# Kernel tuning notes

Hardware: AMD Instinct MI355X
Metric: run time of the kernel (lower is better)

Reference implementation:

```python
import jax, jax.numpy as jnp
import numpy as np

TOPK = 32
NUM_PT = 8192
NUM_KP = 8
HW = 19200


def _conv3(x, w, b):
    # x: [1, C, N], w: [O, C, 3] -> [1, O, N] (padding=1)
    y = jax.lax.conv_general_dilated(x, w, (1,), [(1, 1)],
                                     dimension_numbers=('NCH', 'OIH', 'NCH'))
    return y + b[None, :, None]


def setup_inputs() -> dict:
    key = jax.random.key(0)
    ks = jax.random.split(key, 64)

    def p(i, *shape):
        return (jax.random.normal(ks[i], shape, dtype=jnp.float32) * 0.05)

    inp = {
        'seg': jax.random.uniform(ks[0], (1, NUM_PT), dtype=jnp.float32),
        'img': jax.random.normal(ks[1], (1, 32, HW), dtype=jnp.float32),
        'cloud': jax.random.normal(ks[2], (1, NUM_PT, 3), dtype=jnp.float32),
        't': jax.random.normal(ks[3], (1, 3), dtype=jnp.float32),
        'choose': jax.random.randint(ks[4], (1, 1, NUM_PT), 0, HW),
        # Pseudo3DConv params (all 1x1 conv1d == channel matmul)
        'pconv1_w': p(5, 64, 3),    'pconv1_b': p(6, 64),
        'pconv2_w': p(7, 128, 64),  'pconv2_b': p(8, 128),
        'conv1_w': p(9, 64, 32),    'conv1_b': p(10, 64),
        'conv2_w': p(11, 128, 64),  'conv2_b': p(12, 128),
        'psconv1_w': p(13, 256, 128), 'psconv1_b': p(14, 256),
        'psconv2_w': p(15, 128, 256), 'psconv2_b': p(16, 128),
        'final_w': p(17, 128, 416), 'final_b': p(18, 128),
        # heads
        'seg1_w': p(19, 64, 128, 3), 'seg1_b': p(20, 64),
        'seg2_w': p(21, 32, 64),     'seg2_b': p(22, 32),
        'seg3_w': p(23, 1, 32),      'seg3_b': p(24, 1),
        'dis1_w': p(25, 64, 128, 3), 'dis1_b': p(26, 64),
        'dis2_w': p(27, 32, 64),     'dis2_b': p(28, 32),
        'dis3_w': p(29, 1, 32),      'dis3_b': p(30, 1),
        'lin1_w': p(31, 90, 128),    'lin1_b': p(32, 90),
        'lin2_w': p(33, 64, 90),     'lin2_b': p(34, 64),
        'lin3_w': p(35, 3 * NUM_KP, 64), 'lin3_b': p(36, 3 * NUM_KP),
    }
    return inp


def reference(seg, img, cloud, t, choose,
              pconv1_w, pconv1_b, pconv2_w, pconv2_b,
              conv1_w, conv1_b, conv2_w, conv2_b,
              psconv1_w, psconv1_b, psconv2_w, psconv2_b,
              final_w, final_b,
              seg1_w, seg1_b, seg2_w, seg2_b, seg3_w, seg3_b,
              dis1_w, dis1_b, dis2_w, dis2_b, dis3_w, dis3_b,
              lin1_w, lin1_b, lin2_w, lin2_b, lin3_w, lin3_b):
    lrelu = jax.nn.leaky_relu  # slope 0.01, same as torch default
    N = NUM_PT

    # gather per-point image features at chosen pixels: [N, 32]
    feat = jnp.take(img[0], choose[0, 0], axis=1).T
    c = cloud[0]  # [N, 3]

    # ---- KNN (self included, as in knn_cuda) ----
    d2 = jnp.sum((c[:, None, :] - c[None, :, :]) ** 2, axis=-1)  # [N, N]
    _, idx = jax.lax.top_k(-d2, TOPK)  # [N, K] nearest neighbors

    # ---- point-feature MLP (pconv1 -> lrelu -> pconv2) ----
    pf = lrelu(c @ pconv1_w.T + pconv1_b) @ pconv2_w.T + pconv2_b  # [N, 128]

    # ---- vectorized per-point neighbor gather + MLP + weighted maxpool ----
    nf = feat[idx]    # [N, K, 32]
    npf = pf[idx]     # [N, K, 128]
    npos = c[idx]     # [N, K, 3]
    w = jax.nn.softmax(-jnp.linalg.norm(c[:, None, :] - npos, axis=-1), axis=1)  # [N, K]

    f = lrelu(nf @ conv1_w.T + conv1_b) @ conv2_w.T + conv2_b          # [N, K, 128]
    fp = lrelu(npf @ psconv1_w.T + psconv1_b) @ psconv2_w.T + psconv2_b  # [N, K, 128]
    f = jnp.max(f * w[..., None], axis=1)    # [N, 128]
    fp = jnp.max(fp * w[..., None], axis=1)  # [N, 128]

    # final2 = [fp | img_feat], final1 = [f | cloud_feat] -> cat -> [N, 416]
    final = jnp.concatenate([fp, feat, f, pf], axis=1)
    fused = lrelu(final) @ final_w.T + final_b  # [N, 128]
    fused = fused.T[None]  # [1, 128, N]

    def pw(x, w_, b_):  # 1x1 conv1d on [1, C, N]
        return jnp.einsum('oc,bcn->bon', w_, x) + b_[None, :, None]

    # segmentation head
    h = lrelu(_conv3(fused, seg1_w, seg1_b))
    seg_pre = pw(lrelu(pw(h, seg2_w, seg2_b)), seg3_w, seg3_b).reshape(1, N)

    # distance-to-center weighting (norm along coord dim, softmax over points)
    dis_center = jax.nn.softmax(
        jnp.linalg.norm(cloud - (-t)[:, None, :], axis=2), axis=1)  # [1, N]

    # distance head (on unweighted fused features, matching torch op order)
    h = lrelu(_conv3(fused, dis1_w, dis1_b))
    dis_pre = pw(lrelu(pw(h, dis2_w, dis2_b)), dis3_w, dis3_b).reshape(1, N)

    # weight fused features by center distance and segmentation, sum-pool
    fused = fused * dis_center[:, None, :] * seg[:, None, :]
    g = jnp.sum(fused, axis=2)  # [1, 128]

    kp = lrelu(g @ lin1_w.T + lin1_b)
    kp = lrelu(kp @ lin2_w.T + lin2_b)
    keypoints = (kp @ lin3_w.T + lin3_b).reshape(1, NUM_KP, 3)
    return keypoints, dis_pre, dis_center, seg_pre
```

## Files before the change

### kernel.cpp

```cpp
#include <hip/hip_runtime.h>
#include <math.h>

#define NPT 8192
#define HWIMG 19200
#define KCAP 128

using short8 = __attribute__((ext_vector_type(8))) short;
using short4v = __attribute__((ext_vector_type(4))) short;
using f32x4  = __attribute__((ext_vector_type(4))) float;

__device__ __forceinline__ float lrelu(float x) { return x > 0.f ? x : 0.01f * x; }
__device__ __forceinline__ unsigned short f2bf(float v) {
  unsigned u = __float_as_uint(v);
  return (unsigned short)((u + 0x7fffu + ((u >> 16) & 1u)) >> 16);
}
__device__ __forceinline__ float bf2f(unsigned short h) {
  return __uint_as_float(((unsigned)h) << 16);
}
__device__ __forceinline__ void split2(float v, unsigned short& h, unsigned short& l) {
  h = f2bf(v);
  l = f2bf(v - bf2f(h));
}
__device__ __forceinline__ void mfma3(f32x4& acc, short8 ah, short8 al, short8 wh, short8 wl) {
  acc = __builtin_amdgcn_mfma_f32_16x16x32_bf16(ah, wh, acc, 0, 0, 0);
  acc = __builtin_amdgcn_mfma_f32_16x16x32_bf16(al, wh, acc, 0, 0, 0);
  acc = __builtin_amdgcn_mfma_f32_16x16x32_bf16(ah, wl, acc, 0, 0, 0);
}

__device__ __forceinline__ int swz(int o, int k, int Kc) {
  return ((((o >> 4) * Kc + (k >> 5)) << 6) + (((k >> 3) & 3) << 4) + (o & 15)) * 8 + (k & 7);
}

#define OFF_PCONV2  0
#define OFF_CONV1   8192
#define OFF_CONV2   10240
#define OFF_PSCONV1 18432
#define OFF_PSCONV2 51200
#define OFF_FINAL   83968
#define OFF_W3      137216
#define OFF_W2P     186368

#define S_C4    NPT
#define S_G     129
#define S_BIASC 128
#define S_B2C   64
#define S_FEAT  (NPT*32)
#define S_W3    49152
#define S_W2P   8192
#define S_WSPL  OFF_W3
#define PREP_TOTAL (S_C4 + S_G + S_BIASC + S_B2C + S_FEAT + S_W3 + S_W2P + S_WSPL)
__global__ void k_prep(const float* __restrict__ cloud, const int* __restrict__ choose,
                       const float* __restrict__ img,
                       const float* __restrict__ seg1_w, const float* __restrict__ dis1_w,
                       const float* __restrict__ seg1_b, const float* __restrict__ dis1_b,
                       const float* __restrict__ seg2_w, const float* __restrict__ dis2_w,
                       const float* __restrict__ seg2_b, const float* __restrict__ dis2_b,
                       const float* __restrict__ pconv2_w, const float* __restrict__ conv1_w,
                       const float* __restrict__ conv2_w, const float* __restrict__ psconv1_w,
                       const float* __restrict__ psconv2_w, const float* __restrict__ final_w,
                       float* __restrict__ c4, float* __restrict__ g,
                       float* __restrict__ biasc, float* __restrict__ bias2c,
                       float* __restrict__ feat,
                       unsigned short* __restrict__ feat_h, unsigned short* __restrict__ feat_l,
                       unsigned short* __restrict__ Wh, unsigned short* __restrict__ Wl) {
  int j = blockIdx.x * blockDim.x + threadIdx.x;
  if (j < S_C4) {
    float x = cloud[j*3+0], y = cloud[j*3+1], z = cloud[j*3+2];
    float4 v; v.x = x; v.y = y; v.z = z; v.w = x*x + y*y + z*z;
    ((float4*)c4)[j] = v;
    return;
  }
  j -= S_C4;
  if (j < S_G) { g[j] = 0.f; return; }
  j -= S_G;
  if (j < S_BIASC) { biasc[j] = (j < 64) ? seg1_b[j] : dis1_b[j-64]; return; }
  j -= S_BIASC;
  if (j < S_B2C) { bias2c[j] = (j < 32) ? seg2_b[j] : dis2_b[j-32]; return; }
  j -= S_B2C;
  if (j < S_FEAT) {
    int n = j >> 5, ch = j & 31;
    float v = img[ch*HWIMG + choose[n]];
    feat[j] = v;
    unsigned short hh, ll; split2(v, hh, ll);
    int d = swz(n, ch, 1);
    feat_h[d] = hh; feat_l[d] = ll;
    return;
  }
  j -= S_FEAT;
  if (j < S_W3) {
    int h = j / 24576, r = j - h*24576, o = r / 384, k = r - o*384;
    int t = k >> 7, c = k & 127;
    float v = (h ? dis1_w : seg1_w)[o*384 + c*3 + t];
    unsigned short hh, ll; split2(v, hh, ll);
    int d = OFF_W3 + swz(h*64 + o, k, 12);
    Wh[d] = hh; Wl[d] = ll;
    return;
  }
  j -= S_W3;
  if (j < S_W2P) {
    int o = j >> 7, c = j & 127;
    float v = 0.f;
    if (o < 32) { if (c < 64) v = seg2_w[o*64 + c]; }
    else        { if (c >= 64) v = dis2_w[(o-32)*64 + (c-64)]; }
    unsigned short hh, ll; split2(v, hh, ll);
    int d = OFF_W2P + swz(o, c, 4);
    Wh[d] = hh; Wl[d] = ll;
    return;
  }
  j -= S_W2P;
  if (j < S_WSPL) {
    float v; int d;
    if (j < OFF_CONV1) {
      int o = j >> 6, k = j & 63;
      v = pconv2_w[j]; d = OFF_PCONV2 + swz(o, k, 2);
    } else if (j < OFF_CONV2) {
      int jj = j - OFF_CONV1, o = jj >> 5, k = jj & 31;
      v = conv1_w[jj]; d = OFF_CONV1 + swz(o, k, 1);
    } else if (j < OFF_PSCONV1) {
      int jj = j - OFF_CONV2, o = jj >> 6, k = jj & 63;
      v = conv2_w[jj]; d = OFF_CONV2 + swz(o, k, 2);
    } else if (j < OFF_PSCONV2) {
      int jj = j - OFF_PSCONV1, o = jj >> 7, k = jj & 127;
      v = psconv1_w[jj]; d = OFF_PSCONV1 + swz(o, k, 4);
    } else if (j < OFF_FINAL) {
      int jj = j - OFF_PSCONV2, o = jj >> 8, k = jj & 255;
      v = psconv2_w[jj]; d = OFF_PSCONV2 + swz(o, k, 8);
    } else {
      int jj = j - OFF_FINAL, o = jj / 416, k = jj - o*416;
      v = final_w[jj]; d = OFF_FINAL + swz(o, k, 13);
    }
    unsigned short hh, ll; split2(v, hh, ll);
    Wh[d] = hh; Wl[d] = ll;
  }
}

__device__ __forceinline__ unsigned bsort32u(unsigned key, int lane) {
#pragma unroll
  for (int k = 2; k <= 64; k <<= 1) {
#pragma unroll
    for (int j = k >> 1; j > 0; j >>= 1) {
      unsigned o = __shfl_xor(key, j, 64);
      bool keepmin = (((lane & j) == 0) == ((lane & k) == 0));
      key = ((o < key) == keepmin) ? o : key;
    }
  }
  return key;
}
__device__ __forceinline__ unsigned long long bsort64(unsigned long long key, int lane) {
#pragma unroll
  for (int k = 2; k <= 64; k <<= 1) {
#pragma unroll
    for (int j = k >> 1; j > 0; j >>= 1) {
      unsigned long long o = __shfl_xor(key, j, 64);
      bool keepmin = (((lane & j) == 0) == ((lane & k) == 0));
      bool omin = o < key;
      key = (omin == keepmin) ? o : key;
    }
  }
  return key;
}
__device__ __forceinline__ unsigned long long bmerge64(unsigned long long key, int lane) {
#pragma unroll
  for (int j = 32; j > 0; j >>= 1) {
    unsigned long long o = __shfl_xor(key, j, 64);
    bool keepmin = ((lane & j) == 0);
    bool omin = o < key;
    key = (omin == keepmin) ? o : key;
  }
  return key;
}

#define MEGA_GRID 3073
__global__ __launch_bounds__(256) void k_mega(const float4* __restrict__ c4,
                                              int* __restrict__ idxo, float* __restrict__ wo,
                                              const float* __restrict__ cloud,
                                              const float* __restrict__ tvec,
                                              float* __restrict__ dc,
                                              const float* __restrict__ pconv1_w, const float* __restrict__ pconv1_b,
                                              const float* __restrict__ pconv2_b, const float* __restrict__ psconv1_b,
                                              const float* __restrict__ psconv2_b,
                                              const unsigned short* __restrict__ feat_h,
                                              const unsigned short* __restrict__ feat_l,
                                              const float* __restrict__ conv1_b, const float* __restrict__ conv2_b,
                                              const unsigned short* __restrict__ Wh,
                                              const unsigned short* __restrict__ Wl,
                                              float* __restrict__ pf, float* __restrict__ Yfp,
                                              float* __restrict__ Yf) {
  __shared__ __align__(16) char smem[16384];
  int tid = threadIdx.x, lane = tid & 63, w = tid >> 6;
  int mr = lane & 15, q = lane >> 4;
  if (blockIdx.x > 2048) {
    unsigned short* sh_h = (unsigned short*)smem;
    unsigned short* sh_l = (unsigned short*)(smem + 8192);
    int cb = blockIdx.x - 2049;
    if (cb < 512) {
      int m0 = cb * 16;
      float4 cp = c4[m0 + mr];
      short8 ah0, al0, ah1, al1;
#pragma unroll
      for (int j = 0; j < 8; ++j) {
        int c0 = q*8 + j, c1 = 32 + q*8 + j;
        float v0 = lrelu(fmaf(cp.x, pconv1_w[c0*3+0], fmaf(cp.y, pconv1_w[c0*3+1],
                          fmaf(cp.z, pconv1_w[c0*3+2], pconv1_b[c0]))));
        float v1 = lrelu(fmaf(cp.x, pconv1_w[c1*3+0], fmaf(cp.y, pconv1_w[c1*3+1],
                          fmaf(cp.z, pconv1_w[c1*3+2], pconv1_b[c1]))));
        unsigned short hh, ll;
        split2(v0, hh, ll); ah0[j] = (short)hh; al0[j] = (short)ll;
        split2(v1, hh, ll); ah1[j] = (short)hh; al1[j] = (short)ll;
      }
      f32x4 acc[2];
#pragma unroll
      for (int t = 0; t < 2; ++t) { f32x4 z = {0.f,0.f,0.f,0.f}; acc[t] = z; }
      const unsigned short* W2h = Wh + OFF_PCONV2;
      const unsigned short* W2l = Wl + OFF_PCONV2;
#pragma unroll
      for (int tt = 0; tt < 2; ++tt) {
        int t1 = 2*w + tt;
        int w0 = ((t1*2 + 0)*64 + lane)*8, w1 = ((t1*2 + 1)*64 + lane)*8;
        mfma3(acc[tt], ah0, al0, *(const short8*)(W2h + w0), *(const short8*)(W2l + w0));
        mfma3(acc[tt], ah1, al1, *(const short8*)(W2h + w1), *(const short8*)(W2l + w1));
      }
#pragma unroll
      for (int tt = 0; tt < 2; ++tt) {
        int t1 = 2*w + tt, n = t1*16 + mr;
        float b = pconv2_b[n];
        int ks2 = t1 >> 1, q2 = (t1 & 1)*2 + (mr >> 3), jd = mr & 7;
#pragma unroll
        for (int r = 0; r < 4; ++r) {
          int row = q*4 + r;
          float v = acc[tt][r] + b;
          pf[(size_t)(m0+row)*128 + n] = v;
          unsigned short hh, ll; split2(v, hh, ll);
          int p = ((ks2*16 + row)*4 + q2)*8 + jd;
          sh_h[p] = hh; sh_l[p] = ll;
        }
      }
      __syncthreads();
      f32x4 acc3[2];
#pragma unroll
      for (int t = 0; t < 2; ++t) { f32x4 z = {0.f,0.f,0.f,0.f}; acc3[t] = z; }
      const unsigned short* W3h = Wh + OFF_PSCONV1;
      const unsigned short* W3l = Wl + OFF_PSCONV1;
      const unsigned short* W4h = Wh + OFF_PSCONV2;
      const unsigned short* W4l = Wl + OFF_PSCONV2;
#pragma unroll
      for (int h = 0; h < 2; ++h) {
        f32x4 acc2[2];
#pragma unroll
        for (int t = 0; t < 2; ++t) { f32x4 z = {0.f,0.f,0.f,0.f}; acc2[t] = z; }
#pragma unroll
        for (int ks = 0; ks < 4; ++ks) {
          int ap = ((ks*16 + mr)*4 + q)*8;
          short8 ah = *(const short8*)&sh_h[ap];
          short8 al = *(const short8*)&sh_l[ap];
#pragma unroll
          for (int tt = 0; tt < 2; ++tt) {
            int ts = h*8 + 2*w + tt;
            int wb = ((ts*4 + ks)*64 + lane)*8;
            mfma3(acc2[tt], ah, al, *(const short8*)(W3h + wb), *(const short8*)(W3l + wb));
          }
        }
#pragma unroll
        for (int tt = 0; tt < 2; ++tt) {
          int tl = 2*w + tt;
          int n = h*128 + tl*16 + mr;
          float b = psconv1_b[n];
          int ks3 = tl >> 1, q3 = (tl & 1)*2 + (mr >> 3), jd = mr & 7;
#pragma unroll
          for (int r = 0; r < 4; ++r) {
            int row = q*4 + r;
            float v = lrelu(acc2[tt][r] + b);
            unsigned short hh, ll; split2(v, hh, ll);
            int p = 2048 + ((ks3*16 + row)*4 + q3)*8 + jd;
            sh_h[p] = hh; sh_l[p] = ll;
          }
        }
        __syncthreads();
#pragma unroll
        for (int ks = 0; ks < 4; ++ks) {
          int ap = 2048 + ((ks*16 + mr)*4 + q)*8;
          short8 ah = *(const short8*)&sh_h[ap];
          short8 al = *(const short8*)&sh_l[ap];
#pragma unroll
          for (int tt = 0; tt < 2; ++tt) {
            int wb = (((2*w+tt)*8 + h*4 + ks)*64 + lane)*8;
            mfma3(acc3[tt], ah, al, *(const short8*)(W4h + wb), *(const short8*)(W4l + wb));
          }
        }
        __syncthreads();
      }
#pragma unroll
      for (int tt = 0; tt < 2; ++tt) {
        int n = (2*w+tt)*16 + mr;
        float b = psconv2_b[n];
#pragma unroll
        for (int r = 0; r < 4; ++r)
          Yfp[(size_t)(m0 + q*4 + r)*128 + n] = acc3[tt][r] + b;
      }
    } else {
      int m0 = (cb - 512) * 16;
      int ab = ((m0 >> 4)*64 + lane)*8;
      short8 ah = *(const short8*)(feat_h + ab);
      short8 al = *(const short8*)(feat_l + ab);
      f32x4 acc = {0.f,0.f,0.f,0.f};
      const unsigned short* W1h = Wh + OFF_CONV1;
      const unsigned short* W1l = Wl + OFF_CONV1;
      {
        int wb = (w*64 + lane)*8;
        mfma3(acc, ah, al, *(const short8*)(W1h + wb), *(const short8*)(W1l + wb));
      }
      {
        int n = w*16 + mr;
        float b = conv1_b[n];
        int ks2 = n >> 5, q2 = (n >> 3) & 3, jd = mr & 7;
#pragma unroll
        for (int r = 0; r < 4; ++r) {
          int row = q*4 + r;
          float v = lrelu(acc[r] + b);
          unsigned short hh, ll; split2(v, hh, ll);
          int p = ((ks2*16 + row)*4 + q2)*8 + jd;
          sh_h[p] = hh; sh_l[p] = ll;
        }
      }
      __syncthreads();
      f32x4 acc2[2];
#pragma unroll
      for (int t = 0; t < 2; ++t) { f32x4 z = {0.f,0.f,0.f,0.f}; acc2[t] = z; }
      const unsigned short* W2h = Wh + OFF_CONV2;
      const unsigned short* W2l = Wl + OFF_CONV2;
#pragma unroll
      for (int ks = 0; ks < 2; ++ks) {
        int ap = ((ks*16 + mr)*4 + q)*8;
        short8 a2 = *(const short8*)&sh_h[ap];
        short8 a2l = *(const short8*)&sh_l[ap];
#pragma unroll
        for (int tt = 0; tt < 2; ++tt) {
          int wb = (((2*w+tt)*2 + ks)*64 + lane)*8;
          mfma3(acc2[tt], a2, a2l, *(const short8*)(W2h + wb), *(const short8*)(W2l + wb));
        }
      }
#pragma unroll
      for (int tt = 0; tt < 2; ++tt) {
        int n = (2*w+tt)*16 + mr;
        float b = conv2_b[n];
#pragma unroll
        for (int r = 0; r < 4; ++r)
          Yf[(size_t)(m0 + q*4 + r)*128 + n] = acc2[tt][r] + b;
      }
    }
    return;
  }
  if (blockIdx.x == 2048) {
    float* sred = (float*)smem;
    float tx = tvec[0], ty = tvec[1], tz = tvec[2];
    float v[32];
    float m = -INFINITY;
#pragma unroll
    for (int i2 = 0; i2 < 32; ++i2) {
      int n = i2*256 + tid;
      float ax = cloud[n*3+0] + tx, ay = cloud[n*3+1] + ty, az = cloud[n*3+2] + tz;
      v[i2] = sqrtf(ax*ax + ay*ay + az*az);
      m = fmaxf(m, v[i2]);
    }
#pragma unroll
    for (int o = 1; o < 64; o <<= 1) m = fmaxf(m, __shfl_xor(m, o, 64));
    if (lane == 0) sred[w] = m;
    __syncthreads();
    m = fmaxf(fmaxf(sred[0], sred[1]), fmaxf(sred[2], sred[3]));
    __syncthreads();
    float s = 0.f;
#pragma unroll
    for (int i2 = 0; i2 < 32; ++i2) { v[i2] = expf(v[i2] - m); s += v[i2]; }
#pragma unroll
    for (int o = 1; o < 64; o <<= 1) s += __shfl_xor(s, o, 64);
    if (lane == 0) sred[w] = s;
    __syncthreads();
    s = sred[0] + sred[1] + sred[2] + sred[3];
#pragma unroll
    for (int i2 = 0; i2 < 32; ++i2) dc[i2*256 + tid] = v[i2] / s;
    return;
  }
  float (*smin)[256] = (float(*)[256])smem;
  float* sTv = (float*)(smem + 4096);
  int*   scnt = (int*)(smem + 4112);
  float (*sd)[KCAP] = (float(*)[KCAP])(smem + 4128);
  int   (*sj)[KCAP] = (int(*)[KCAP])(smem + 6176);
  int q0 = blockIdx.x * 4;
  float4 p0 = c4[q0], p1 = c4[q0+1], p2 = c4[q0+2], p3 = c4[q0+3];
  float p0x = -2.f*p0.x, p0y = -2.f*p0.y, p0z = -2.f*p0.z;
  float p1x = -2.f*p1.x, p1y = -2.f*p1.y, p1z = -2.f*p1.z;
  float p2x = -2.f*p2.x, p2y = -2.f*p2.y, p2z = -2.f*p2.z;
  float p3x = -2.f*p3.x, p3y = -2.f*p3.y, p3z = -2.f*p3.z;
#define DDOT(PX,PY,PZ,PW,CJ) fmaf(PX,(CJ).x, fmaf(PY,(CJ).y, fmaf(PZ,(CJ).z, PW + (CJ).w)))
  float m0 = INFINITY, m1 = INFINITY, m2 = INFINITY, m3 = INFINITY;
  for (int t = 0; t < 32; t += 2) {
    float4 ca = c4[t*256 + tid];
    float4 cb = c4[t*256 + 256 + tid];
    float a0 = DDOT(p0x,p0y,p0z,p0.w,ca), b0 = DDOT(p0x,p0y,p0z,p0.w,cb);
    float a1 = DDOT(p1x,p1y,p1z,p1.w,ca), b1 = DDOT(p1x,p1y,p1z,p1.w,cb);
    float a2 = DDOT(p2x,p2y,p2z,p2.w,ca), b2 = DDOT(p2x,p2y,p2z,p2.w,cb);
    float a3 = DDOT(p3x,p3y,p3z,p3.w,ca), b3 = DDOT(p3x,p3y,p3z,p3.w,cb);
    m0 = fminf(m0, fminf(a0, b0));
    m1 = fminf(m1, fminf(a1, b1));
    m2 = fminf(m2, fminf(a2, b2));
    m3 = fminf(m3, fminf(a3, b3));
  }
  smin[0][tid] = m0; smin[1][tid] = m1; smin[2][tid] = m2; smin[3][tid] = m3;
  if (tid < 4) scnt[tid] = 0;
  __syncthreads();
  {
    float4 vv = *(const float4*)&smin[w][lane*4];
    float m4 = fmaxf(fminf(fminf(vv.x, vv.y), fminf(vv.z, vv.w)), 0.f);
    unsigned key = bsort32u(__float_as_uint(m4), lane);
    float T = __uint_as_float(__shfl(key, 31, 64));
    if (lane == 0) sTv[w] = T * (1.f + 2e-5f) + 4e-5f;
  }
  __syncthreads();
  float T0 = sTv[0], T1 = sTv[1], T2 = sTv[2], T3 = sTv[3];
  for (int t = 0; t < 32; ++t) {
    int j = t*256 + tid;
    float4 cj = c4[j];
    float d;
#define APPEND(Q, P) { \
    float dx_ = (P).x-cj.x, dy_ = (P).y-cj.y, dz_ = (P).z-cj.z; \
    float de_ = dx_*dx_ + dy_*dy_ + dz_*dz_; \
    int p_ = atomicAdd(&scnt[Q],1); if (p_ < KCAP) { sd[Q][p_] = de_; sj[Q][p_] = j; } }
    d = DDOT(p0x,p0y,p0z,p0.w,cj); if (d <= T0) APPEND(0, p0);
    d = DDOT(p1x,p1y,p1z,p1.w,cj); if (d <= T1) APPEND(1, p1);
    d = DDOT(p2x,p2y,p2z,p2.w,cj); if (d <= T2) APPEND(2, p2);
    d = DDOT(p3x,p3y,p3z,p3.w,cj); if (d <= T3) APPEND(3, p3);
  }
  __syncthreads();
  int M = scnt[w]; if (M > KCAP) M = KCAP;
  unsigned long long key = (lane < M)
      ? (((unsigned long long)__float_as_uint(sd[w][lane]) << 32) | (unsigned)sj[w][lane])
      : ~0ull;
  key = bsort64(key, lane);
  for (int base = 64; base < M; base += 64) {
    unsigned long long nk = (base + lane < M)
        ? (((unsigned long long)__float_as_uint(sd[w][base+lane]) << 32) | (unsigned)sj[w][base+lane])
        : ~0ull;
    nk = bsort64(nk, lane);
    nk = __shfl_xor(nk, 63, 64);
    key = key < nk ? key : nk;
    key = bmerge64(key, lane);
  }
  float dsel = __uint_as_float((unsigned)(key >> 32));
  int   jsel = (int)(unsigned)(key & 0xffffffffu);
  float v = -sqrtf(dsel);
  float mx = v;
#pragma unroll
  for (int o = 1; o < 32; o <<= 1) mx = fmaxf(mx, __shfl_xor(mx, o, 64));
  float e = expf(v - mx);
  float s = e;
#pragma unroll
  for (int o = 1; o < 32; o <<= 1) s += __shfl_xor(s, o, 64);
  if (lane < 32) {
    int qd = q0 + w;
    wo[qd*32 + lane] = e / s;
    idxo[qd*32 + lane] = jsel;
  }
}

__global__ __launch_bounds__(256) void k_tail(const float* __restrict__ Yf,
                                              const float* __restrict__ Yfp,
                                              const float* __restrict__ feat,
                                              const float* __restrict__ pf,
                                              const int* __restrict__ idx,
                                              const float* __restrict__ wsm,
                                              const unsigned short* __restrict__ Wh,
                                              const unsigned short* __restrict__ Wl,
                                              const float* __restrict__ final_b,
                                              const float* __restrict__ biasc,
                                              const float* __restrict__ bias2c,
                                              const float* __restrict__ segw, const float* __restrict__ segb,
                                              const float* __restrict__ disw, const float* __restrict__ disb,
                                              const float* __restrict__ dcw, const float* __restrict__ segin,
                                              float* __restrict__ g,
                                              float* __restrict__ osegp, float* __restrict__ odisp) {
  __shared__ int sjn[18][32];
  __shared__ float swn[18][32];
  __shared__ __align__(16) char sbuf[37440];
  int tid = threadIdx.x, lane = tid & 63, w = tid >> 6;
  int mr = lane & 15, q = lane >> 4;
  int mt = blockIdx.x, m0 = mt * 16;
  for (int t = tid; t < 18*32; t += 256) {
    int lr = t >> 5, k = t & 31, gr = m0 - 1 + lr;
    if (gr >= 0 && gr < NPT) { sjn[lr][k] = idx[gr*32+k]; swn[lr][k] = wsm[gr*32+k]; }
    else { sjn[lr][k] = 0; swn[lr][k] = 0.f; }
  }
  __syncthreads();
  for (int t = tid; t < 1872; t += 256) {
    int lr, col;
    float4 v4;
    if (t < 1152) {
      lr = t >> 6; int arr = (t >> 5) & 1, cg = t & 31;
      const float* Y = arr ? Yf : Yfp;
      float4 vv[32];
#pragma unroll
      for (int k = 0; k < 32; ++k)
        vv[k] = *(const float4*)&Y[(size_t)sjn[lr][k]*128 + cg*4];
      float ax = -INFINITY, ay = -INFINITY, az = -INFINITY, aw = -INFINITY;
#pragma unroll
      for (int k = 0; k < 32; ++k) {
        float wk = swn[lr][k];
        ax = fmaxf(ax, wk*vv[k].x); ay = fmaxf(ay, wk*vv[k].y);
        az = fmaxf(az, wk*vv[k].z); aw = fmaxf(aw, wk*vv[k].w);
      }
      v4.x = lrelu(ax); v4.y = lrelu(ay); v4.z = lrelu(az); v4.w = lrelu(aw);
      col = (arr ? 160 : 0) + cg*4;
    } else if (t < 1728) {
      int u = t - 1152; lr = u >> 5; int cg = u & 31;
      int gr = m0 - 1 + lr;
      int gc = gr < 0 ? 0 : (gr >= NPT ? NPT-1 : gr);
      float4 p4 = *(const float4*)&pf[(size_t)gc*128 + cg*4];
      v4.x = lrelu(p4.x); v4.y = lrelu(p4.y); v4.z = lrelu(p4.z); v4.w = lrelu(p4.w);
      col = 288 + cg*4;
    } else {
      int u = t - 1728; lr = u >> 3; int cg = u & 7;
      int gr = m0 - 1 + lr;
      int gc = gr < 0 ? 0 : (gr >= NPT ? NPT-1 : gr);
      float4 p4 = *(const float4*)&feat[(size_t)gc*32 + cg*4];
      v4.x = lrelu(p4.x); v4.y = lrelu(p4.y); v4.z = lrelu(p4.z); v4.w = lrelu(p4.w);
      col = 128 + cg*4;
    }
    int gr = m0 - 1 + lr;
    if (gr < 0 || gr >= NPT) { v4.x = 0.f; v4.y = 0.f; v4.z = 0.f; v4.w = 0.f; }
    int ks = col >> 5, qq = (col >> 3) & 3, j0 = col & 7;
    char* base = sbuf + (ks*18 + lr)*80 + qq*16 + j0*2;
    short4v hv, lv;
    unsigned short hh, ll;
    split2(v4.x, hh, ll); hv[0] = (short)hh; lv[0] = (short)ll;
    split2(v4.y, hh, ll); hv[1] = (short)hh; lv[1] = (short)ll;
    split2(v4.z, hh, ll); hv[2] = (short)hh; lv[2] = (short)ll;
    split2(v4.w, hh, ll); hv[3] = (short)hh; lv[3] = (short)ll;
    *(short4v*)base = hv;
    *(short4v*)(base + 18720) = lv;
  }
  __syncthreads();
  f32x4 accA[2], accB[2];
#pragma unroll
  for (int t = 0; t < 2; ++t) {
    f32x4 z = {0.f,0.f,0.f,0.f}; accA[t] = z; accB[t] = z;
  }
  const unsigned short* WFh = Wh + OFF_FINAL;
  const unsigned short* WFl = Wl + OFF_FINAL;
#pragma unroll
  for (int ks = 0; ks < 13; ++ks) {
    int arB = 16 + mr; if (arB > 17) arB = 17;
    const char* pA = sbuf + (ks*18 + mr)*80 + q*16;
    const char* pB = sbuf + (ks*18 + arB)*80 + q*16;
    short8 ahA = *(const short8*)pA;
    short8 alA = *(const short8*)(pA + 18720);
    short8 ahB = *(const short8*)pB;
    short8 alB = *(const short8*)(pB + 18720);
#pragma unroll
    for (int tt = 0; tt < 2; ++tt) {
      int wb = (((2*w+tt)*13 + ks)*64 + lane)*8;
      short8 wh = *(const short8*)(WFh + wb);
      short8 wl = *(const short8*)(WFl + wb);
      mfma3(accA[tt], ahA, alA, wh, wl);
      mfma3(accB[tt], ahB, alB, wh, wl);
    }
  }
  __syncthreads();
#pragma unroll
  for (int tile = 0; tile < 2; ++tile) {
#pragma unroll
    for (int tt = 0; tt < 2; ++tt) {
      int t2 = 2*w + tt, n = t2*16 + mr;
      float b = final_b[n];
      int ksA = t2 >> 1, qq = (t2 & 1)*2 + (mr >> 3), jd = mr & 7;
#pragma unroll
      for (int r = 0; r < 4; ++r) {
        int lr = tile*16 + q*4 + r;
        if (lr > 17) continue;
        int gr = m0 - 1 + lr;
        float v = (tile ? accB[tt][r] : accA[tt][r]) + b;
        if (gr < 0 || gr >= NPT) v = 0.f;
        unsigned short hh, ll; split2(v, hh, ll);
        char* p = sbuf + (ksA*18 + lr)*80 + qq*16 + jd*2;
        *(unsigned short*)p = hh;
        *(unsigned short*)(p + 5760) = ll;
      }
    }
  }
  __syncthreads();
  {
    int ks2 = tid >> 6, q2 = (tid >> 4) & 3, mr2 = tid & 15;
    int lr = mr2 + 1;
    const char* p = sbuf + (ks2*18 + lr)*80 + q2*16;
    short8 oh = *(const short8*)p;
    short8 ol = *(const short8*)(p + 5760);
    int gr = m0 + mr2;
    float wrow = dcw[gr] * segin[gr];
    float* sred = (float*)(sbuf + 26112);
#pragma unroll
    for (int j = 0; j < 8; ++j)
      sred[tid*8 + j] = (bf2f((unsigned short)oh[j]) + bf2f((unsigned short)ol[j])) * wrow;
  }
  __syncthreads();
  if (tid < 128) {
    float* sred = (float*)(sbuf + 26112);
    int ks = tid >> 5, q2 = (tid >> 3) & 3, j = tid & 7;
    float s = 0.f;
#pragma unroll
    for (int mr2 = 0; mr2 < 16; ++mr2) s += sred[((ks << 6) + (q2 << 4) + mr2)*8 + j];
    atomicAdd(&g[tid], s);
  }
  f32x4 acc3[2];
#pragma unroll
  for (int t = 0; t < 2; ++t) { f32x4 z = {0.f,0.f,0.f,0.f}; acc3[t] = z; }
  const unsigned short* W3h = Wh + OFF_W3;
  const unsigned short* W3l = Wl + OFF_W3;
#pragma unroll
  for (int ks = 0; ks < 12; ++ks) {
    int tap = ks >> 2, ksA = ks & 3;
    int ar = mr + tap;
    const char* p = sbuf + (ksA*18 + ar)*80 + q*16;
    short8 ah = *(const short8*)p;
    short8 al = *(const short8*)(p + 5760);
#pragma unroll
    for (int tt = 0; tt < 2; ++tt) {
      int wb = (((2*w+tt)*12 + ks)*64 + lane)*8;
      mfma3(acc3[tt], ah, al, *(const short8*)(W3h + wb), *(const short8*)(W3l + wb));
    }
  }
#pragma unroll
  for (int tt = 0; tt < 2; ++tt) {
    int t2 = 2*w + tt, n = t2*16 + mr;
    float b = biasc[n];
    int ks2 = t2 >> 1, q2 = (t2 & 1)*2 + (mr >> 3), jd = mr & 7;
#pragma unroll
    for (int r = 0; r < 4; ++r) {
      int row = q*4 + r;
      float v = lrelu(acc3[tt][r] + b);
      unsigned short hh, ll; split2(v, hh, ll);
      char* p = sbuf + 11520 + (ks2*16 + row)*80 + q2*16 + jd*2;
      *(unsigned short*)p = hh;
      *(unsigned short*)(p + 5120) = ll;
    }
  }
  __syncthreads();
  f32x4 acc4 = {0.f,0.f,0.f,0.f};
  const unsigned short* WPh = Wh + OFF_W2P;
  const unsigned short* WPl = Wl + OFF_W2P;
#pragma unroll
  for (int ks = 0; ks < 4; ++ks) {
    const char* p = sbuf + 11520 + (ks*16 + mr)*80 + q*16;
    short8 ah = *(const short8*)p;
    short8 al = *(const short8*)(p + 5120);
    int wb = ((w*4 + ks)*64 + lane)*8;
    mfma3(acc4, ah, al, *(const short8*)(WPh + wb), *(const short8*)(WPl + wb));
  }
  float hw = (w < 2) ? segw[w*16 + mr] : disw[(w-2)*16 + mr];
  float bb = bias2c[w*16 + mr];
  float* shead = (float*)(sbuf + 21760);
#pragma unroll
  for (int r = 0; r < 4; ++r)
    shead[(w*16 + q*4 + r)*17 + mr] = lrelu(acc4[r] + bb) * hw;
  __syncthreads();
  if (tid < 16) {
    float a = 0.f;
#pragma unroll
    for (int i = 0; i < 16; ++i) a += shead[(tid)*17 + i] + shead[(16 + tid)*17 + i];
    osegp[m0 + tid] = a + segb[0];
  } else if (tid < 32) {
    int r2 = tid - 16;
    float a = 0.f;
#pragma unroll
    for (int i = 0; i < 16; ++i) a += shead[(32 + r2)*17 + i] + shead[(48 + r2)*17 + i];
    odisp[m0 + r2] = a + disb[0];
  }
}

__global__ void k_kp(const float* __restrict__ g,
                     const float* __restrict__ l1w, const float* __restrict__ l1b,
                     const float* __restrict__ l2w, const float* __restrict__ l2b,
                     const float* __restrict__ l3w, const float* __restrict__ l3b,
                     float* __restrict__ o_kp) {
  __shared__ float sg[128], s1[90], s2[64];
  int tid = threadIdx.x;
  if (tid < 128) sg[tid] = g[tid];
  __syncthreads();
  if (tid < 90) {
    float a = l1b[tid];
    for (int i = 0; i < 128; ++i) a += sg[i]*l1w[tid*128+i];
    s1[tid] = lrelu(a);
  }
  __syncthreads();
  if (tid < 64) {
    float a = l2b[tid];
    for (int i = 0; i < 90; ++i) a += s1[i]*l2w[tid*90+i];
    s2[tid] = lrelu(a);
  }
  __syncthreads();
  if (tid < 24) {
    float a = l3b[tid];
    for (int i = 0; i < 64; ++i) a += s2[i]*l3w[tid*64+i];
    o_kp[tid] = a;
  }
}

extern "C" void kernel_launch(void* const* d_in, const int* in_sizes, int n_in,
                              void* d_out, int out_size, void* d_ws, size_t ws_size,
                              hipStream_t stream) {
  const float* seg      = (const float*)d_in[0];
  const float* img      = (const float*)d_in[1];
  const float* cloud    = (const float*)d_in[2];
  const float* tvec     = (const float*)d_in[3];
  const int*   choose   = (const int*)d_in[4];
  const float* pconv1_w = (const float*)d_in[5];
  const float* pconv1_b = (const float*)d_in[6];
  const float* pconv2_w = (const float*)d_in[7];
  const float* pconv2_b = (const float*)d_in[8];
  const float* conv1_w  = (const float*)d_in[9];
  const float* conv1_b  = (const float*)d_in[10];
  const float* conv2_w  = (const float*)d_in[11];
  const float* conv2_b  = (const float*)d_in[12];
  const float* psconv1_w= (const float*)d_in[13];
  const float* psconv1_b= (const float*)d_in[14];
  const float* psconv2_w= (const float*)d_in[15];
  const float* psconv2_b= (const float*)d_in[16];
  const float* final_w  = (const float*)d_in[17];
  const float* final_b  = (const float*)d_in[18];
  const float* seg1_w   = (const float*)d_in[19];
  const float* seg1_b   = (const float*)d_in[20];
  const float* seg2_w   = (const float*)d_in[21];
  const float* seg2_b   = (const float*)d_in[22];
  const float* seg3_w   = (const float*)d_in[23];
  const float* seg3_b   = (const float*)d_in[24];
  const float* dis1_w   = (const float*)d_in[25];
  const float* dis1_b   = (const float*)d_in[26];
  const float* dis2_w   = (const float*)d_in[27];
  const float* dis2_b   = (const float*)d_in[28];
  const float* dis3_w   = (const float*)d_in[29];
  const float* dis3_b   = (const float*)d_in[30];
  const float* lin1_w   = (const float*)d_in[31];
  const float* lin1_b   = (const float*)d_in[32];
  const float* lin2_w   = (const float*)d_in[33];
  const float* lin2_b   = (const float*)d_in[34];
  const float* lin3_w   = (const float*)d_in[35];
  const float* lin3_b   = (const float*)d_in[36];

  float* out = (float*)d_out;
  float* ws  = (float*)d_ws;

  float* c4     = ws + 0;
  float* feat   = ws + 32768;
  unsigned short* feat_h = (unsigned short*)(ws + 294912);
  unsigned short* feat_l = (unsigned short*)(ws + 425984);
  float* pf     = ws + 557056;
  float* Yf     = ws + 1605632;
  float* Yfp    = ws + 2654208;
  int*   idx    = (int*)(ws + 3702784);
  float* wsm    = ws + 3964928;
  unsigned short* Wh    = (unsigned short*)(ws + 9732096);
  unsigned short* Wl    = (unsigned short*)(ws + 9829376);
  float* biasc  = ws + 9926656;
  float* bias2c = ws + 9926784;
  float* g      = ws + 9926848;

  float* o_kp   = out;
  float* o_disp = out + 24;
  float* o_dc   = out + 8216;
  float* o_segp = out + 16408;

  k_prep<<<(PREP_TOTAL + 255)/256, 256, 0, stream>>>(
      cloud, choose, img, seg1_w, dis1_w, seg1_b, dis1_b,
      seg2_w, dis2_w, seg2_b, dis2_b,
      pconv2_w, conv1_w, conv2_w, psconv1_w, psconv2_w, final_w,
      c4, g, biasc, bias2c, feat, feat_h, feat_l, Wh, Wl);

  k_mega<<<MEGA_GRID, 256, 0, stream>>>(
      (const float4*)c4, idx, wsm, cloud, tvec, o_dc,
      pconv1_w, pconv1_b, pconv2_b, psconv1_b, psconv2_b,
      feat_h, feat_l, conv1_b, conv2_b, Wh, Wl, pf, Yfp, Yf);

  k_tail<<<512, 256, 0, stream>>>(
      Yf, Yfp, feat, pf, idx, wsm, Wh, Wl,
      final_b, biasc, bias2c, seg3_w, seg3_b, dis3_w, dis3_b,
      o_dc, seg, g,
      o_segp, o_disp);

  k_kp<<<1, 128, 0, stream>>>(g, lin1_w, lin1_b, lin2_w, lin2_b,
                              lin3_w, lin3_b, o_kp);

  (void)in_sizes; (void)n_in; (void)out_size; (void)ws_size;
}
```

Baseline: 232.9 us.

## Process eight queries per block in kNN with SoA cloud and packed float2 math

The kNN part of the fused kernel now handles 8 query points per block instead of 4, halving the number of kNN blocks. It reads the cloud from a new structure-of-arrays copy written in the prep kernel, using float2 loads and packed FMA/min so each load is reused across more queries. The cost is more registers per thread and a longer per-block selection phase, where each wave now sorts two queries.

```diff
diff --git a/kernel.cpp b/kernel.cpp
--- a/kernel.cpp
+++ b/kernel.cpp
@@ -8,6 +8,7 @@
 using short8 = __attribute__((ext_vector_type(8))) short;
 using short4v = __attribute__((ext_vector_type(4))) short;
 using f32x4  = __attribute__((ext_vector_type(4))) float;
+using f32x2  = __attribute__((ext_vector_type(2))) float;
 
 __device__ __forceinline__ float lrelu(float x) { return x > 0.f ? x : 0.01f * x; }
 __device__ __forceinline__ unsigned short f2bf(float v) {
@@ -58,7 +59,8 @@
                        const float* __restrict__ pconv2_w, const float* __restrict__ conv1_w,
                        const float* __restrict__ conv2_w, const float* __restrict__ psconv1_w,
                        const float* __restrict__ psconv2_w, const float* __restrict__ final_w,
-                       float* __restrict__ c4, float* __restrict__ g,
+                       float* __restrict__ c4, float* __restrict__ soa,
+                       float* __restrict__ g,
                        float* __restrict__ biasc, float* __restrict__ bias2c,
                        float* __restrict__ feat,
                        unsigned short* __restrict__ feat_h, unsigned short* __restrict__ feat_l,
@@ -68,6 +70,7 @@
     float x = cloud[j*3+0], y = cloud[j*3+1], z = cloud[j*3+2];
     float4 v; v.x = x; v.y = y; v.z = z; v.w = x*x + y*y + z*z;
     ((float4*)c4)[j] = v;
+    soa[j] = x; soa[NPT + j] = y; soa[2*NPT + j] = z; soa[3*NPT + j] = v.w;
     return;
   }
   j -= S_C4;
@@ -170,8 +173,9 @@
   return key;
 }
 
-#define MEGA_GRID 3073
+#define MEGA_GRID 2049
 __global__ __launch_bounds__(256) void k_mega(const float4* __restrict__ c4,
+                                              const float* __restrict__ soa,
                                               int* __restrict__ idxo, float* __restrict__ wo,
                                               const float* __restrict__ cloud,
                                               const float* __restrict__ tvec,
@@ -189,10 +193,10 @@
   __shared__ __align__(16) char smem[16384];
   int tid = threadIdx.x, lane = tid & 63, w = tid >> 6;
   int mr = lane & 15, q = lane >> 4;
-  if (blockIdx.x > 2048) {
+  if (blockIdx.x > 1024) {
     unsigned short* sh_h = (unsigned short*)smem;
     unsigned short* sh_l = (unsigned short*)(smem + 8192);
-    int cb = blockIdx.x - 2049;
+    int cb = blockIdx.x - 1025;
     if (cb < 512) {
       int m0 = cb * 16;
       float4 cp = c4[m0 + mr];
@@ -350,7 +354,7 @@
     }
     return;
   }
-  if (blockIdx.x == 2048) {
+  if (blockIdx.x == 1024) {
     float* sred = (float*)smem;
     float tx = tvec[0], ty = tvec[1], tz = tvec[2];
     float v[32];
@@ -381,84 +385,110 @@
     return;
   }
   float (*smin)[256] = (float(*)[256])smem;
-  float* sTv = (float*)(smem + 4096);
-  int*   scnt = (int*)(smem + 4112);
-  float (*sd)[KCAP] = (float(*)[KCAP])(smem + 4128);
-  int   (*sj)[KCAP] = (int(*)[KCAP])(smem + 6176);
-  int q0 = blockIdx.x * 4;
-  float4 p0 = c4[q0], p1 = c4[q0+1], p2 = c4[q0+2], p3 = c4[q0+3];
-  float p0x = -2.f*p0.x, p0y = -2.f*p0.y, p0z = -2.f*p0.z;
-  float p1x = -2.f*p1.x, p1y = -2.f*p1.y, p1z = -2.f*p1.z;
-  float p2x = -2.f*p2.x, p2y = -2.f*p2.y, p2z = -2.f*p2.z;
-  float p3x = -2.f*p3.x, p3y = -2.f*p3.y, p3z = -2.f*p3.z;
-#define DDOT(PX,PY,PZ,PW,CJ) fmaf(PX,(CJ).x, fmaf(PY,(CJ).y, fmaf(PZ,(CJ).z, PW + (CJ).w)))
-  float m0 = INFINITY, m1 = INFINITY, m2 = INFINITY, m3 = INFINITY;
-  for (int t = 0; t < 32; t += 2) {
-    float4 ca = c4[t*256 + tid];
-    float4 cb = c4[t*256 + 256 + tid];
-    float a0 = DDOT(p0x,p0y,p0z,p0.w,ca), b0 = DDOT(p0x,p0y,p0z,p0.w,cb);
-    float a1 = DDOT(p1x,p1y,p1z,p1.w,ca), b1 = DDOT(p1x,p1y,p1z,p1.w,cb);
-    float a2 = DDOT(p2x,p2y,p2z,p2.w,ca), b2 = DDOT(p2x,p2y,p2z,p2.w,cb);
-    float a3 = DDOT(p3x,p3y,p3z,p3.w,ca), b3 = DDOT(p3x,p3y,p3z,p3.w,cb);
-    m0 = fminf(m0, fminf(a0, b0));
-    m1 = fminf(m1, fminf(a1, b1));
-    m2 = fminf(m2, fminf(a2, b2));
-    m3 = fminf(m3, fminf(a3, b3));
-  }
-  smin[0][tid] = m0; smin[1][tid] = m1; smin[2][tid] = m2; smin[3][tid] = m3;
-  if (tid < 4) scnt[tid] = 0;
-  __syncthreads();
-  {
-    float4 vv = *(const float4*)&smin[w][lane*4];
+  float (*sd)[KCAP] = (float(*)[KCAP])smem;
+  int   (*sj)[KCAP] = (int(*)[KCAP])(smem + 4096);
+  float* sTv = (float*)(smem + 8192);
+  int*   scnt = (int*)(smem + 8224);
+  const float* cx = soa;
+  const float* cy = soa + NPT;
+  const float* cz = soa + 2*NPT;
+  const float* cw = soa + 3*NPT;
+  int q0 = blockIdx.x * 8;
+  float4 P[8];
+#pragma unroll
+  for (int i = 0; i < 8; ++i) P[i] = c4[q0 + i];
+  f32x2 QX[8], QY[8], QZ[8], QW[8];
+#pragma unroll
+  for (int i = 0; i < 8; ++i) {
+    QX[i][0] = QX[i][1] = -2.f*P[i].x;
+    QY[i][0] = QY[i][1] = -2.f*P[i].y;
+    QZ[i][0] = QZ[i][1] = -2.f*P[i].z;
+    QW[i][0] = QW[i][1] = P[i].w;
+  }
+#define PDOT(QXI,QYI,QZI,QWI) \
+  __builtin_elementwise_fma(X, QXI, __builtin_elementwise_fma(Yv, QYI, \
+    __builtin_elementwise_fma(Z, QZI, Wv + QWI)))
+  f32x2 inf2 = {INFINITY, INFINITY};
+  f32x2 mv[8];
+#pragma unroll
+  for (int i = 0; i < 8; ++i) mv[i] = inf2;
+  for (int t = 0; t < 16; ++t) {
+    int j = t*512 + tid*2;
+    f32x2 X  = *(const f32x2*)&cx[j];
+    f32x2 Yv = *(const f32x2*)&cy[j];
+    f32x2 Z  = *(const f32x2*)&cz[j];
+    f32x2 Wv = *(const f32x2*)&cw[j];
+#pragma unroll
+    for (int i = 0; i < 8; ++i)
+      mv[i] = __builtin_elementwise_min(mv[i], PDOT(QX[i],QY[i],QZ[i],QW[i]));
+  }
+#pragma unroll
+  for (int i = 0; i < 8; ++i) smin[i][tid] = fminf(mv[i][0], mv[i][1]);
+  if (tid < 8) scnt[tid] = 0;
+  __syncthreads();
+#pragma unroll
+  for (int u = 0; u < 2; ++u) {
+    int qq = w*2 + u;
+    float4 vv = *(const float4*)&smin[qq][lane*4];
     float m4 = fmaxf(fminf(fminf(vv.x, vv.y), fminf(vv.z, vv.w)), 0.f);
     unsigned key = bsort32u(__float_as_uint(m4), lane);
     float T = __uint_as_float(__shfl(key, 31, 64));
-    if (lane == 0) sTv[w] = T * (1.f + 2e-5f) + 4e-5f;
-  }
-  __syncthreads();
-  float T0 = sTv[0], T1 = sTv[1], T2 = sTv[2], T3 = sTv[3];
-  for (int t = 0; t < 32; ++t) {
-    int j = t*256 + tid;
-    float4 cj = c4[j];
-    float d;
-#define APPEND(Q, P) { \
-    float dx_ = (P).x-cj.x, dy_ = (P).y-cj.y, dz_ = (P).z-cj.z; \
+    if (lane == 0) sTv[qq] = T * (1.f + 2e-5f) + 4e-5f;
+  }
+  __syncthreads();
+  float Tq[8];
+#pragma unroll
+  for (int i = 0; i < 8; ++i) Tq[i] = sTv[i];
+#define APPEND8(Q, PQ, XX, YY, ZZ, J) { \
+    float dx_ = (PQ).x-(XX), dy_ = (PQ).y-(YY), dz_ = (PQ).z-(ZZ); \
     float de_ = dx_*dx_ + dy_*dy_ + dz_*dz_; \
-    int p_ = atomicAdd(&scnt[Q],1); if (p_ < KCAP) { sd[Q][p_] = de_; sj[Q][p_] = j; } }
-    d = DDOT(p0x,p0y,p0z,p0.w,cj); if (d <= T0) APPEND(0, p0);
-    d = DDOT(p1x,p1y,p1z,p1.w,cj); if (d <= T1) APPEND(1, p1);
-    d = DDOT(p2x,p2y,p2z,p2.w,cj); if (d <= T2) APPEND(2, p2);
-    d = DDOT(p3x,p3y,p3z,p3.w,cj); if (d <= T3) APPEND(3, p3);
-  }
-  __syncthreads();
-  int M = scnt[w]; if (M > KCAP) M = KCAP;
-  unsigned long long key = (lane < M)
-      ? (((unsigned long long)__float_as_uint(sd[w][lane]) << 32) | (unsigned)sj[w][lane])
-      : ~0ull;
-  key = bsort64(key, lane);
-  for (int base = 64; base < M; base += 64) {
-    unsigned long long nk = (base + lane < M)
-        ? (((unsigned long long)__float_as_uint(sd[w][base+lane]) << 32) | (unsigned)sj[w][base+lane])
+    int p_ = atomicAdd(&scnt[Q],1); if (p_ < KCAP) { sd[Q][p_] = de_; sj[Q][p_] = (J); } }
+  for (int t = 0; t < 16; ++t) {
+    int j = t*512 + tid*2;
+    f32x2 X  = *(const f32x2*)&cx[j];
+    f32x2 Yv = *(const f32x2*)&cy[j];
+    f32x2 Z  = *(const f32x2*)&cz[j];
+    f32x2 Wv = *(const f32x2*)&cw[j];
+#pragma unroll
+    for (int i = 0; i < 8; ++i) {
+      f32x2 d = PDOT(QX[i],QY[i],QZ[i],QW[i]);
+      if (d[0] <= Tq[i]) APPEND8(i, P[i], X[0], Yv[0], Z[0], j);
+      if (d[1] <= Tq[i]) APPEND8(i, P[i], X[1], Yv[1], Z[1], j+1);
+    }
+  }
+  __syncthreads();
+#pragma unroll
+  for (int u = 0; u < 2; ++u) {
+    int qq = w*2 + u;
+    int M = scnt[qq]; if (M > KCAP) M = KCAP;
+    unsigned long long key = (lane < M)
+        ? (((unsigned long long)__float_as_uint(sd[qq][lane]) << 32) | (unsigned)sj[qq][lane])
         : ~0ull;
-    nk = bsort64(nk, lane);
-    nk = __shfl_xor(nk, 63, 64);
-    key = key < nk ? key : nk;
-    key = bmerge64(key, lane);
-  }
-  float dsel = __uint_as_float((unsigned)(key >> 32));
-  int   jsel = (int)(unsigned)(key & 0xffffffffu);
-  float v = -sqrtf(dsel);
-  float mx = v;
-#pragma unroll
-  for (int o = 1; o < 32; o <<= 1) mx = fmaxf(mx, __shfl_xor(mx, o, 64));
-  float e = expf(v - mx);
-  float s = e;
-#pragma unroll
-  for (int o = 1; o < 32; o <<= 1) s += __shfl_xor(s, o, 64);
-  if (lane < 32) {
-    int qd = q0 + w;
-    wo[qd*32 + lane] = e / s;
-    idxo[qd*32 + lane] = jsel;
+    key = bsort64(key, lane);
+    for (int base = 64; base < M; base += 64) {
+      unsigned long long nk = (base + lane < M)
+          ? (((unsigned long long)__float_as_uint(sd[qq][base+lane]) << 32) | (unsigned)sj[qq][base+lane])
+          : ~0ull;
+      nk = bsort64(nk, lane);
+      nk = __shfl_xor(nk, 63, 64);
+      key = key < nk ? key : nk;
+      key = bmerge64(key, lane);
+    }
+    float dsel = __uint_as_float((unsigned)(key >> 32));
+    int   jsel = (int)(unsigned)(key & 0xffffffffu);
+    float v = -sqrtf(dsel);
+    float mx = v;
+#pragma unroll
+    for (int o = 1; o < 32; o <<= 1) mx = fmaxf(mx, __shfl_xor(mx, o, 64));
+    float e = expf(v - mx);
+    float s = e;
+#pragma unroll
+    for (int o = 1; o < 32; o <<= 1) s += __shfl_xor(s, o, 64);
+    if (lane < 32) {
+      int qd = q0 + qq;
+      wo[qd*32 + lane] = e / s;
+      idxo[qd*32 + lane] = jsel;
+    }
   }
 }
 
@@ -755,6 +785,7 @@
   float* Yfp    = ws + 2654208;
   int*   idx    = (int*)(ws + 3702784);
   float* wsm    = ws + 3964928;
+  float* soa    = ws + 4227072;
   unsigned short* Wh    = (unsigned short*)(ws + 9732096);
   unsigned short* Wl    = (unsigned short*)(ws + 9829376);
   float* biasc  = ws + 9926656;
@@ -770,10 +801,10 @@
       cloud, choose, img, seg1_w, dis1_w, seg1_b, dis1_b,
       seg2_w, dis2_w, seg2_b, dis2_b,
       pconv2_w, conv1_w, conv2_w, psconv1_w, psconv2_w, final_w,
-      c4, g, biasc, bias2c, feat, feat_h, feat_l, Wh, Wl);
+      c4, soa, g, biasc, bias2c, feat, feat_h, feat_l, Wh, Wl);
 
   k_mega<<<MEGA_GRID, 256, 0, stream>>>(
-      (const float4*)c4, idx, wsm, cloud, tvec, o_dc,
+      (const float4*)c4, soa, idx, wsm, cloud, tvec, o_dc,
       pconv1_w, pconv1_b, pconv2_b, psconv1_b, psconv2_b,
       feat_h, feat_l, conv1_b, conv2_b, Wh, Wl, pf, Yfp, Yf);
 
```

Result: no change. 228.5 us (-1.9%).
